# Kernel optimization log

Hardware: AMD Instinct MI355X
Metric: run time of the kernel (lower is better)

## Reference

```python
import jax, jax.numpy as jnp
import numpy as np
from jax import lax

N_WIRES = 4
# Deterministic stand-in for tq.RandomLayer(n_ops=50): fixed gate sequence.
_rng = np.random.RandomState(12345)
_GATES = ['rx', 'ry', 'rz', 'crx', 'cnot']
RAND_SPEC = []
for _ in range(50):
    g = _GATES[_rng.randint(len(_GATES))]
    if g in ('crx', 'cnot'):
        w = [int(v) for v in _rng.choice(N_WIRES, size=2, replace=False)]
    else:
        w = [int(_rng.randint(N_WIRES))]
    RAND_SPEC.append((g, w))
N_RAND_PARAMS = sum(1 for g, _ in RAND_SPEC if g != 'cnot')

C64 = jnp.complex64
H_MAT = (jnp.array([[1, 1], [1, -1]], C64) / np.float32(np.sqrt(2.0)))
SX_MAT = 0.5 * jnp.array([[1 + 1j, 1 - 1j], [1 - 1j, 1 + 1j]], C64)
CNOT_MAT = jnp.array([[1, 0, 0, 0], [0, 1, 0, 0], [0, 0, 0, 1], [0, 0, 1, 0]], C64)


def rx_mat(t):
    t = jnp.asarray(t, jnp.float32)
    c = jnp.cos(t / 2).astype(C64)
    js = (-1j) * jnp.sin(t / 2).astype(C64)
    return jnp.stack([jnp.stack([c, js], -1), jnp.stack([js, c], -1)], -2)


def ry_mat(t):
    t = jnp.asarray(t, jnp.float32)
    c = jnp.cos(t / 2).astype(C64)
    s = jnp.sin(t / 2).astype(C64)
    return jnp.stack([jnp.stack([c, -s], -1), jnp.stack([s, c], -1)], -2)


def rz_mat(t):
    t = jnp.asarray(t, jnp.float32).astype(C64)
    em = jnp.exp(-0.5j * t)
    ep = jnp.exp(0.5j * t)
    z = jnp.zeros_like(em)
    return jnp.stack([jnp.stack([em, z], -1), jnp.stack([z, ep], -1)], -2)


def crx_mat(t):
    r = rx_mat(t)  # [2,2]
    m = jnp.eye(4, dtype=C64)
    return m.at[2:, 2:].set(r)


def apply_1q(state, U, wire):
    # state: [B,2,2,2,2]; U: [2,2] or [B,2,2]
    st = jnp.moveaxis(state, wire + 1, 1)
    sh = st.shape
    st = st.reshape(sh[0], 2, -1)
    if U.ndim == 2:
        st = jnp.einsum('ij,bjk->bik', U, st)
    else:
        st = jnp.einsum('bij,bjk->bik', U, st)
    return jnp.moveaxis(st.reshape(sh), 1, wire + 1)


def apply_2q(state, U, w0, w1):
    # U: [4,4], basis |w0 w1>
    st = jnp.moveaxis(state, (w0 + 1, w1 + 1), (1, 2))
    sh = st.shape
    st = st.reshape(sh[0], 4, -1)
    st = jnp.einsum('ij,bjk->bik', U, st)
    return jnp.moveaxis(st.reshape(sh), (1, 2), (w0 + 1, w1 + 1))


def maxpool2(h):
    return lax.reduce_window(h, -jnp.inf, lax.max, (1, 1, 2, 2), (1, 1, 2, 2), 'VALID')


def conv2d_same(h, w, b):
    o = lax.conv_general_dilated(h, w, (1, 1), 'SAME', dimension_numbers=('NCHW', 'OIHW', 'NCHW'))
    return o + b[None, :, None, None]


def setup_inputs() -> dict:
    key = jax.random.key(0)
    ks = jax.random.split(key, 12)
    B = 8192
    inp = {}
    inp['x'] = jax.random.normal(ks[0], (B, 1, 28, 28), jnp.float32)
    inp['conv1_w'] = jax.random.normal(ks[1], (8, 1, 3, 3), jnp.float32) * 0.2
    inp['conv1_b'] = jax.random.normal(ks[2], (8,), jnp.float32) * 0.05
    inp['conv2_w'] = jax.random.normal(ks[3], (16, 8, 3, 3), jnp.float32) * 0.1
    inp['conv2_b'] = jax.random.normal(ks[4], (16,), jnp.float32) * 0.05
    inp['gate_params'] = jax.random.normal(ks[5], (4,), jnp.float32)  # rx0, ry0, rz0, crx0
    inp['rand_params'] = jax.random.normal(ks[6], (N_RAND_PARAMS,), jnp.float32)
    inp['bn_gamma'] = jnp.ones((4,), jnp.float32)
    inp['bn_beta'] = jnp.zeros((4,), jnp.float32)
    inp['fc_w'] = jax.random.normal(ks[7], (1, 4), jnp.float32) * 0.5
    inp['fc_b'] = jnp.zeros((1,), jnp.float32)
    return inp


def reference(x, conv1_w, conv1_b, conv2_w, conv2_b, gate_params, rand_params, bn_gamma, bn_beta, fc_w, fc_b):
    B = x.shape[0]
    # --- CNN feature extractor ---
    h = jax.nn.relu(conv2d_same(x, conv1_w, conv1_b))
    h = maxpool2(h)                       # [B,8,14,14]
    h = jax.nn.relu(conv2d_same(h, conv2_w, conv2_b))
    h = maxpool2(h)                       # [B,16,7,7]
    pooled = h.mean(axis=(2, 3))          # [B,16] -> rotation angles

    # --- quantum circuit on 4 wires, state [B,2,2,2,2], wire 0 = axis 1 ---
    state = jnp.zeros((B, 2, 2, 2, 2), C64).at[:, 0, 0, 0, 0].set(1.0)

    # GeneralEncoder '4x4_ryzxy': ry, rz, rx, ry over wires 0..3 with inputs 0..15
    idx = 0
    for f in (ry_mat, rz_mat, rx_mat, ry_mat):
        for w in range(N_WIRES):
            state = apply_1q(state, f(pooled[:, idx]), w)
            idx += 1

    # RandomLayer (frozen deterministic 50-op sequence)
    mat_of = {'rx': rx_mat, 'ry': ry_mat, 'rz': rz_mat}
    p = 0
    for g, wires in RAND_SPEC:
        if g == 'cnot':
            state = apply_2q(state, CNOT_MAT, wires[0], wires[1])
        elif g == 'crx':
            state = apply_2q(state, crx_mat(rand_params[p]), wires[0], wires[1])
            p += 1
        else:
            state = apply_1q(state, mat_of[g](rand_params[p]), wires[0])
            p += 1

    # fixed trainable gates + fixed gates
    state = apply_1q(state, rx_mat(gate_params[0]), 0)
    state = apply_1q(state, ry_mat(gate_params[1]), 1)
    state = apply_1q(state, rz_mat(gate_params[2]), 3)
    state = apply_2q(state, crx_mat(gate_params[3]), 0, 2)
    state = apply_1q(state, H_MAT, 3)
    state = apply_1q(state, SX_MAT, 2)
    state = apply_2q(state, CNOT_MAT, 3, 0)

    # MeasureAll(PauliZ): <Z_w> = p(bit_w=0) - p(bit_w=1)
    probs = state.real ** 2 + state.imag ** 2  # [B,2,2,2,2]
    zvec = jnp.array([1.0, -1.0], jnp.float32)
    exps = []
    for w in range(N_WIRES):
        pw = probs.sum(axis=tuple(a for a in range(1, 5) if a != w + 1))  # [B,2]
        exps.append(pw @ zvec)
    out = jnp.stack(exps, axis=1)  # [B,4]

    # BatchNorm1d (training-mode batch statistics, eps=1e-5)
    mu = out.mean(axis=0)
    var = out.var(axis=0)
    out = (out - mu) / jnp.sqrt(var + 1e-5) * bn_gamma + bn_beta

    # Linear classifier 4 -> 1
    return out @ fc_w.T + fc_b
```

## Files before the change

### kernel.cpp

```cpp
#include <hip/hip_runtime.h>
#include <hip/hip_bf16.h>
#include <hip/hip_fp16.h>
#include <cstdint>
#include <random>

typedef __attribute__((ext_vector_type(8))) short short8;
typedef __attribute__((ext_vector_type(4))) float floatx4;

#define NGMAX 60
struct GateSpec {
  unsigned char type[NGMAX];
  unsigned char w0[NGMAX];
  unsigned char w1[NGMAX];
  signed char   src[NGMAX];
  signed char   pidx[NGMAX];
  int n;
};

static GateSpec build_spec() {
  GateSpec sp; sp.n = 0;
  std::mt19937 mt(12345u);
  int p = 0;
  auto add = [&](int ty, int a, int b, int s, int pi) {
    sp.type[sp.n] = (unsigned char)ty; sp.w0[sp.n] = (unsigned char)a;
    sp.w1[sp.n] = (unsigned char)b; sp.src[sp.n] = (signed char)s;
    sp.pidx[sp.n] = (signed char)pi; sp.n++;
  };
  for (int op = 0; op < 50; ++op) {
    unsigned g;
    for (;;) { uint32_t v = mt() & 7u; if (v <= 4u) { g = v; break; } }
    if (g == 3u || g == 4u) {
      int arr[4] = {0, 1, 2, 3};
      for (int i = 3; i >= 1; --i) {
        uint32_t mask = (i == 1) ? 1u : 3u;
        uint32_t j;
        for (;;) { j = mt() & mask; if (j <= (uint32_t)i) break; }
        int t = arr[i]; arr[i] = arr[j]; arr[j] = t;
      }
      if (g == 3u) add(3, arr[0], arr[1], 0, p++);
      else         add(4, arr[0], arr[1], 2, -1);
    } else {
      int w = (int)(mt() & 3u);
      add((int)g, w, 0, 0, p++);
    }
  }
  add(0, 0, 0, 1, 0);
  add(1, 1, 0, 1, 1);
  add(2, 3, 0, 1, 2);
  add(3, 0, 2, 1, 3);
  add(5, 3, 0, 2, -1);
  add(6, 2, 0, 2, -1);
  add(4, 3, 0, 2, -1);
  return sp;
}

__device__ __forceinline__ float2 cmul(float2 a, float2 b) {
  return make_float2(fmaf(a.x, b.x, -a.y * b.y), fmaf(a.x, b.y, a.y * b.x));
}

__device__ __forceinline__ unsigned short f2bf(float f) {
  __hip_bfloat16 h = __float2bfloat16(f);
  return *reinterpret_cast<unsigned short*>(&h);
}

#define WS_BW   512
#define WS_W1C  1408
#define WS_O4   1456

__global__ void prep_kernel(const float* __restrict__ rp, const float* __restrict__ gp,
                            const float* __restrict__ c1w, const float* __restrict__ c1b,
                            const float* __restrict__ c2w,
                            float* __restrict__ ws, GateSpec sp) {
  const int tid = threadIdx.x;

  __hip_bfloat16* Bwg = (__hip_bfloat16*)(ws + WS_BW);
  __half2* w1cg = (__half2*)(ws + WS_W1C);
  for (int i = tid; i < 896; i += 256)
    ((unsigned int*)Bwg)[i] = 0u;
  __syncthreads();
  for (int i = tid; i < 1152; i += 256) {
    const int co = i / 72, rem = i - co * 72;
    const int ci = rem / 9, tap = rem - ci * 9;
    Bwg[co * 112 + tap * 8 + ci] = __float2bfloat16(c2w[i]);
  }
  if (tid < 40) {
    const int p = tid / 10, t = tid - p * 10;
    __half2 v;
    if (t < 9) v = __halves2half2(__float2half(c1w[(2 * p) * 9 + t]),
                                  __float2half(c1w[(2 * p + 1) * 9 + t]));
    else       v = __halves2half2(__float2half(c1b[2 * p]), __float2half(c1b[2 * p + 1]));
    w1cg[p * 12 + t] = v;
  }

  const int r = tid & 15;
  const int c = tid >> 4;
  float2 u = make_float2((r == c) ? 1.f : 0.f, 0.f);
  for (int g = 0; g < sp.n; ++g) {
    const int ty = sp.type[g];
    float th = 0.f;
    const int s = sp.src[g];
    if (s == 0) th = rp[(int)sp.pidx[g]];
    else if (s == 1) th = gp[(int)sp.pidx[g]];
    const float ch = cosf(th * 0.5f), sh = sinf(th * 0.5f);
    if (ty == 0) {
      const int m = 1 << (3 - sp.w0[g]);
      const float px_ = __shfl_xor(u.x, m), py_ = __shfl_xor(u.y, m);
      u = make_float2(fmaf(ch, u.x, sh * py_), fmaf(ch, u.y, -sh * px_));
    } else if (ty == 1) {
      const int bp = 3 - sp.w0[g]; const int m = 1 << bp; const int b = (r >> bp) & 1;
      const float px_ = __shfl_xor(u.x, m), py_ = __shfl_xor(u.y, m);
      const float sgn = b ? sh : -sh;
      u = make_float2(fmaf(ch, u.x, sgn * px_), fmaf(ch, u.y, sgn * py_));
    } else if (ty == 2) {
      const int bp = 3 - sp.w0[g]; const int b = (r >> bp) & 1;
      u = cmul(make_float2(ch, b ? sh : -sh), u);
    } else if (ty == 3) {
      const int bpc = 3 - sp.w0[g]; const int m = 1 << (3 - sp.w1[g]);
      const float px_ = __shfl_xor(u.x, m), py_ = __shfl_xor(u.y, m);
      if ((r >> bpc) & 1)
        u = make_float2(fmaf(ch, u.x, sh * py_), fmaf(ch, u.y, -sh * px_));
    } else if (ty == 4) {
      const int bpc = 3 - sp.w0[g]; const int m = 1 << (3 - sp.w1[g]);
      const float px_ = __shfl_xor(u.x, m), py_ = __shfl_xor(u.y, m);
      if ((r >> bpc) & 1) u = make_float2(px_, py_);
    } else if (ty == 5) {
      const int bp = 3 - sp.w0[g]; const int m = 1 << bp; const int b = (r >> bp) & 1;
      const float px_ = __shfl_xor(u.x, m), py_ = __shfl_xor(u.y, m);
      const float is2 = 0.70710678118654752f;
      u = b ? make_float2(is2 * (px_ - u.x), is2 * (py_ - u.y))
            : make_float2(is2 * (u.x + px_), is2 * (u.y + py_));
    } else {
      const int m = 1 << (3 - sp.w0[g]);
      const float px_ = __shfl_xor(u.x, m), py_ = __shfl_xor(u.y, m);
      u = make_float2(0.5f * (u.x - u.y + px_ + py_), 0.5f * (u.x + u.y + py_ - px_));
    }
  }
  ws[2 * (r * 16 + c) + 0] = u.x;
  ws[2 * (r * 16 + c) + 1] = u.y;
}

__global__ __launch_bounds__(256, 4) void cnn_quantum_kernel(
    const float* __restrict__ x,
    const float* __restrict__ c2b,
    const float* __restrict__ ws,
    float* __restrict__ o4, int B) {
  __shared__ __align__(16) __half2 sxp2[4 * 900];
  __shared__ __align__(16) unsigned short h1t[4 * 304 * 8];

  const int tid  = threadIdx.x;
  const int lane = tid & 63;
  const int wid  = tid >> 6;
  int img = blockIdx.x * 4 + wid;
  if (img >= B) img = B - 1;

  const float* __restrict__ Ug = ws;
  const __hip_bfloat16* __restrict__ Bwg = (const __hip_bfloat16*)(ws + WS_BW);
  const __half2* __restrict__ w1cg = (const __half2*)(ws + WS_W1C);

  __half2* swave = sxp2 + wid * 900;
  unsigned short* hwave = h1t + wid * 304 * 8;

  for (int i = lane; i < 116; i += 64) {
    int idx;
    if (i < 30) idx = i;
    else if (i < 60) idx = 870 + (i - 30);
    else { const int r = (i - 60) >> 1, c = (i - 60) & 1; idx = (r + 1) * 30 + (c ? 29 : 0); }
    swave[idx] = __float2half2_rn(0.f);
  }
  {
    const uint4 z4 = make_uint4(0u, 0u, 0u, 0u);
    uint4* h4 = (uint4*)hwave;
    for (int s = lane; s < 304; s += 64) h4[s] = z4;
  }
  const float* xb = x + (size_t)img * 784;
  for (int t = lane; t < 196; t += 64) {
    const float4 v4 = *(const float4*)(xb + 4 * t);
    const int yy = t / 7;
    const int xoff = 4 * (t - 7 * yy);
    __half2* dst = &swave[(yy + 1) * 30 + xoff + 1];
    dst[0] = __float2half2_rn(v4.x);
    dst[1] = __float2half2_rn(v4.y);
    dst[2] = __float2half2_rn(v4.z);
    dst[3] = __float2half2_rn(v4.w);
  }
  __syncthreads();

  {
    const int p = lane & 3;
    const int grp = lane >> 2;
    const __half2* __restrict__ wrow = w1cg + p * 12;
    __half2 wr[9];
#pragma unroll
    for (int k = 0; k < 9; ++k) wr[k] = wrow[k];
    const __half2 bias = wrow[9];
    for (int s = grp; s < 196; s += 16) {
      const int py = s / 14, px = s - py * 14;
      const int base = 2 * (py * 30 + px);
      __half2 q[4][4];
#pragma unroll
      for (int j = 0; j < 4; ++j) {
        const __half2* rowp = &swave[base + j * 30];
        q[j][0] = rowp[0]; q[j][1] = rowp[1]; q[j][2] = rowp[2]; q[j][3] = rowp[3];
      }
      __half2 s00 = bias, s01 = bias, s10 = bias, s11 = bias;
#pragma unroll
      for (int ky = 0; ky < 3; ++ky)
#pragma unroll
        for (int kx = 0; kx < 3; ++kx) {
          const __half2 w = wr[ky * 3 + kx];
          s00 = __hfma2(q[ky][kx], w, s00);
          s01 = __hfma2(q[ky][kx + 1], w, s01);
          s10 = __hfma2(q[ky + 1][kx], w, s10);
          s11 = __hfma2(q[ky + 1][kx + 1], w, s11);
        }
      const float lo = fmaxf(fmaxf(fmaxf(__low2float(s00), __low2float(s01)),
                                   fmaxf(__low2float(s10), __low2float(s11))), 0.f);
      const float hi = fmaxf(fmaxf(fmaxf(__high2float(s00), __high2float(s01)),
                                   fmaxf(__high2float(s10), __high2float(s11))), 0.f);
      const int site = (py + 1) * 16 + (px + 1);
      const unsigned int pk = (unsigned int)f2bf(lo) | ((unsigned int)f2bf(hi) << 16);
      *(unsigned int*)&hwave[site * 8 + 2 * p] = pk;
    }
  }
  __syncthreads();

  float asum = 0.f;
  {
    const int n = lane & 15;
    const int g = lane >> 4;

    short8 bfrag[3];
#pragma unroll
    for (int kt = 0; kt < 3; ++kt)
      bfrag[kt] = *(const short8*)&Bwg[n * 112 + kt * 32 + g * 8];
    const float bias2 = c2b[n];

    for (int t = 0; t < 13; ++t) {
      const int m = lane & 15;
      const int S = t * 16 + m;
      const int p = S >> 2, q = S & 3;
      const int p7 = p / 7;
      const int py = 2 * p7 + (q >> 1);
      const int px = 2 * (p - 7 * p7) + (q & 1);
      floatx4 acc = {0.f, 0.f, 0.f, 0.f};
#pragma unroll
      for (int kt = 0; kt < 3; ++kt) {
        const int tap = kt * 4 + g;
        const int dy = tap / 3, dx = tap - 3 * dy;
        const short8 a = *(const short8*)&hwave[((py + dy) * 16 + (px + dx)) * 8];
        acc = __builtin_amdgcn_mfma_f32_16x16x32_bf16(a, bfrag[kt], acc, 0, 0, 0);
      }
      const int pq = t * 4 + g;
      if (pq < 49) {
        const float v = fmaxf(fmaxf(acc[0], acc[1]), fmaxf(acc[2], acc[3]));
        asum += fmaxf(v + bias2, 0.f);
      }
    }
    asum += __shfl_xor(asum, 16);
    asum += __shfl_xor(asum, 32);
  }

  const float angw = asum * (1.0f / 49.0f);

  const int w = lane & 3;
  const float a0 = __shfl(angw, w);
  const float a1 = __shfl(angw, 4 + w);
  const float a2 = __shfl(angw, 8 + w);
  const float a3 = __shfl(angw, 12 + w);
  float c0, s0; sincosf(a0 * 0.5f, &s0, &c0);
  float2 v0 = make_float2(c0, 0.f), v1 = make_float2(s0, 0.f);
  float c1, s1; sincosf(a1 * 0.5f, &s1, &c1);
  v0 = cmul(make_float2(c1, -s1), v0);
  v1 = cmul(make_float2(c1, s1), v1);
  float c2, s2; sincosf(a2 * 0.5f, &s2, &c2);
  const float2 iv0 = make_float2(-v0.y, v0.x);
  const float2 iv1 = make_float2(-v1.y, v1.x);
  const float2 nv0 = make_float2(c2 * v0.x - s2 * iv1.x, c2 * v0.y - s2 * iv1.y);
  const float2 nv1 = make_float2(c2 * v1.x - s2 * iv0.x, c2 * v1.y - s2 * iv0.y);
  float c3, s3; sincosf(a3 * 0.5f, &s3, &c3);
  v0 = make_float2(c3 * nv0.x - s3 * nv1.x, c3 * nv0.y - s3 * nv1.y);
  v1 = make_float2(s3 * nv0.x + c3 * nv1.x, s3 * nv0.y + c3 * nv1.y);

  const int t16 = lane & 15;
  float2 psi = make_float2(1.f, 0.f);
#pragma unroll
  for (int ww = 0; ww < 4; ++ww) {
    const float g0x = __shfl(v0.x, ww), g0y = __shfl(v0.y, ww);
    const float g1x = __shfl(v1.x, ww), g1y = __shfl(v1.y, ww);
    const int bb = (t16 >> (3 - ww)) & 1;
    const float2 vw = bb ? make_float2(g1x, g1y) : make_float2(g0x, g0y);
    psi = cmul(psi, vw);
  }

  const float2* __restrict__ Uc = (const float2*)Ug;
  float2 accp = make_float2(0.f, 0.f);
#pragma unroll
  for (int j = 0; j < 16; ++j) {
    const float2 uu = Uc[t16 * 16 + j];
    const float ppx = __shfl(psi.x, j), ppy = __shfl(psi.y, j);
    accp.x = fmaf(uu.x, ppx, accp.x); accp.x = fmaf(-uu.y, ppy, accp.x);
    accp.y = fmaf(uu.x, ppy, accp.y); accp.y = fmaf(uu.y, ppx, accp.y);
  }
  const float pr = accp.x * accp.x + accp.y * accp.y;

  float e0 = (t16 & 8) ? -pr : pr;
  float e1 = (t16 & 4) ? -pr : pr;
  float e2 = (t16 & 2) ? -pr : pr;
  float e3 = (t16 & 1) ? -pr : pr;
#pragma unroll
  for (int m = 1; m <= 8; m <<= 1) {
    e0 += __shfl_xor(e0, m); e1 += __shfl_xor(e1, m);
    e2 += __shfl_xor(e2, m); e3 += __shfl_xor(e3, m);
  }
  if (lane == 0) {
    float4 r; r.x = e0; r.y = e1; r.z = e2; r.w = e3;
    *(float4*)(o4 + (size_t)img * 4) = r;
  }
}

__global__ __launch_bounds__(1024) void bn_fc_kernel(
    const float* __restrict__ o4, const float* __restrict__ gamma,
    const float* __restrict__ beta, const float* __restrict__ fcw,
    const float* __restrict__ fcb, float* __restrict__ out, int B) {
  __shared__ float redS[16][8];
  __shared__ float coef[5];
  const int tid = threadIdx.x;
  float s0 = 0, s1 = 0, s2 = 0, s3 = 0, q0 = 0, q1 = 0, q2 = 0, q3 = 0;
  for (int r = tid; r < B; r += 1024) {
    const float4 v = *(const float4*)(o4 + (size_t)r * 4);
    s0 += v.x; s1 += v.y; s2 += v.z; s3 += v.w;
    q0 += v.x * v.x; q1 += v.y * v.y; q2 += v.z * v.z; q3 += v.w * v.w;
  }
#pragma unroll
  for (int off = 32; off > 0; off >>= 1) {
    s0 += __shfl_down(s0, off); s1 += __shfl_down(s1, off);
    s2 += __shfl_down(s2, off); s3 += __shfl_down(s3, off);
    q0 += __shfl_down(q0, off); q1 += __shfl_down(q1, off);
    q2 += __shfl_down(q2, off); q3 += __shfl_down(q3, off);
  }
  const int wv = tid >> 6, ln = tid & 63;
  if (ln == 0) {
    redS[wv][0] = s0; redS[wv][1] = s1; redS[wv][2] = s2; redS[wv][3] = s3;
    redS[wv][4] = q0; redS[wv][5] = q1; redS[wv][6] = q2; redS[wv][7] = q3;
  }
  __syncthreads();
  if (tid == 0) {
    float S[8] = {0, 0, 0, 0, 0, 0, 0, 0};
    for (int w = 0; w < 16; ++w)
      for (int k = 0; k < 8; ++k) S[k] += redS[w][k];
    float C = fcb[0];
    for (int k = 0; k < 4; ++k) {
      const float mu = S[k] / (float)B;
      const float var = S[4 + k] / (float)B - mu * mu;
      const float rstd = 1.0f / sqrtf(var + 1e-5f);
      coef[k] = fcw[k] * gamma[k] * rstd;
      C += fcw[k] * (beta[k] - mu * rstd * gamma[k]);
    }
    coef[4] = C;
  }
  __syncthreads();
  const float A0 = coef[0], A1 = coef[1], A2 = coef[2], A3 = coef[3], Cc = coef[4];
  const int r = blockIdx.x * 256 + tid;
  if (tid < 256 && r < B) {
    const float4 v = *(const float4*)(o4 + (size_t)r * 4);
    out[r] = Cc + A0 * v.x + A1 * v.y + A2 * v.z + A3 * v.w;
  }
}

extern "C" void kernel_launch(void* const* d_in, const int* in_sizes, int n_in,
                              void* d_out, int out_size, void* d_ws, size_t ws_size,
                              hipStream_t stream) {
  const float* x   = (const float*)d_in[0];
  const float* c1w = (const float*)d_in[1];
  const float* c1b = (const float*)d_in[2];
  const float* c2w = (const float*)d_in[3];
  const float* c2b = (const float*)d_in[4];
  const float* gp  = (const float*)d_in[5];
  const float* rp  = (const float*)d_in[6];
  const float* gam = (const float*)d_in[7];
  const float* bet = (const float*)d_in[8];
  const float* fcw = (const float*)d_in[9];
  const float* fcb = (const float*)d_in[10];
  float* out = (float*)d_out;
  const int B = in_sizes[0] / 784;

  float* ws = (float*)d_ws;
  float* o4 = ws + WS_O4;

  GateSpec sp = build_spec();
  prep_kernel<<<1, 256, 0, stream>>>(rp, gp, c1w, c1b, c2w, ws, sp);
  const int nblk = (B + 3) / 4;
  cnn_quantum_kernel<<<nblk, 256, 0, stream>>>(x, c2b, ws, o4, B);
  const int nfin = (B + 255) / 256;
  bn_fc_kernel<<<nfin, 1024, 0, stream>>>(o4, gam, bet, fcw, fcb, out, B);
}
```

Before: 148.7 us.

## Fuse batchnorm and classifier into main kernel via last-block ticket

Removes the separate bn_fc kernel launch and folds its work into the main CNN/quantum kernel. Each block increments an atomic ticket counter after writing its outputs, and the last block to finish computes the batch statistics and the final linear outputs for the whole batch. This saves one kernel launch and its gap. In exchange, the final reduction and output pass run serially on a single 256-thread block instead of many 1024-thread blocks, which could be slow for a large batch.

```diff
diff --git a/kernel.cpp b/kernel.cpp
--- a/kernel.cpp
+++ b/kernel.cpp
@@ -65,13 +65,16 @@
 
 #define WS_BW   512
 #define WS_W1C  1408
-#define WS_O4   1456
+#define WS_TKT  1456
+#define WS_O4   1460
 
 __global__ void prep_kernel(const float* __restrict__ rp, const float* __restrict__ gp,
                             const float* __restrict__ c1w, const float* __restrict__ c1b,
                             const float* __restrict__ c2w,
                             float* __restrict__ ws, GateSpec sp) {
   const int tid = threadIdx.x;
+
+  if (tid == 0) *(int*)(ws + WS_TKT) = 0;
 
   __hip_bfloat16* Bwg = (__hip_bfloat16*)(ws + WS_BW);
   __half2* w1cg = (__half2*)(ws + WS_W1C);
@@ -142,10 +145,16 @@
 __global__ __launch_bounds__(256, 4) void cnn_quantum_kernel(
     const float* __restrict__ x,
     const float* __restrict__ c2b,
-    const float* __restrict__ ws,
-    float* __restrict__ o4, int B) {
+    float* __restrict__ ws,
+    float* __restrict__ o4,
+    const float* __restrict__ gamma, const float* __restrict__ beta,
+    const float* __restrict__ fcw, const float* __restrict__ fcb,
+    float* __restrict__ out, int B) {
   __shared__ __align__(16) __half2 sxp2[4 * 900];
   __shared__ __align__(16) unsigned short h1t[4 * 304 * 8];
+  __shared__ int lastFlag;
+  __shared__ float redS[4][8];
+  __shared__ float coef[5];
 
   const int tid  = threadIdx.x;
   const int lane = tid & 63;
@@ -316,54 +325,55 @@
     float4 r; r.x = e0; r.y = e1; r.z = e2; r.w = e3;
     *(float4*)(o4 + (size_t)img * 4) = r;
   }
-}
-
-__global__ __launch_bounds__(1024) void bn_fc_kernel(
-    const float* __restrict__ o4, const float* __restrict__ gamma,
-    const float* __restrict__ beta, const float* __restrict__ fcw,
-    const float* __restrict__ fcb, float* __restrict__ out, int B) {
-  __shared__ float redS[16][8];
-  __shared__ float coef[5];
-  const int tid = threadIdx.x;
-  float s0 = 0, s1 = 0, s2 = 0, s3 = 0, q0 = 0, q1 = 0, q2 = 0, q3 = 0;
-  for (int r = tid; r < B; r += 1024) {
-    const float4 v = *(const float4*)(o4 + (size_t)r * 4);
-    s0 += v.x; s1 += v.y; s2 += v.z; s3 += v.w;
-    q0 += v.x * v.x; q1 += v.y * v.y; q2 += v.z * v.z; q3 += v.w * v.w;
-  }
-#pragma unroll
-  for (int off = 32; off > 0; off >>= 1) {
-    s0 += __shfl_down(s0, off); s1 += __shfl_down(s1, off);
-    s2 += __shfl_down(s2, off); s3 += __shfl_down(s3, off);
-    q0 += __shfl_down(q0, off); q1 += __shfl_down(q1, off);
-    q2 += __shfl_down(q2, off); q3 += __shfl_down(q3, off);
-  }
-  const int wv = tid >> 6, ln = tid & 63;
-  if (ln == 0) {
-    redS[wv][0] = s0; redS[wv][1] = s1; redS[wv][2] = s2; redS[wv][3] = s3;
-    redS[wv][4] = q0; redS[wv][5] = q1; redS[wv][6] = q2; redS[wv][7] = q3;
-  }
+
   __syncthreads();
   if (tid == 0) {
-    float S[8] = {0, 0, 0, 0, 0, 0, 0, 0};
-    for (int w = 0; w < 16; ++w)
-      for (int k = 0; k < 8; ++k) S[k] += redS[w][k];
-    float C = fcb[0];
-    for (int k = 0; k < 4; ++k) {
-      const float mu = S[k] / (float)B;
-      const float var = S[4 + k] / (float)B - mu * mu;
-      const float rstd = 1.0f / sqrtf(var + 1e-5f);
-      coef[k] = fcw[k] * gamma[k] * rstd;
-      C += fcw[k] * (beta[k] - mu * rstd * gamma[k]);
-    }
-    coef[4] = C;
+    __threadfence();
+    int* tkt = (int*)(ws + WS_TKT);
+    const int ticket = atomicAdd(tkt, 1);
+    lastFlag = (ticket == (int)gridDim.x - 1);
+    if (lastFlag) __threadfence();
   }
   __syncthreads();
-  const float A0 = coef[0], A1 = coef[1], A2 = coef[2], A3 = coef[3], Cc = coef[4];
-  const int r = blockIdx.x * 256 + tid;
-  if (tid < 256 && r < B) {
-    const float4 v = *(const float4*)(o4 + (size_t)r * 4);
-    out[r] = Cc + A0 * v.x + A1 * v.y + A2 * v.z + A3 * v.w;
+  if (lastFlag) {
+    float s0 = 0, s1 = 0, s2 = 0, s3 = 0, q0 = 0, q1 = 0, q2 = 0, q3 = 0;
+    for (int r = tid; r < B; r += 256) {
+      const float4 v = *(const float4*)(o4 + (size_t)r * 4);
+      s0 += v.x; s1 += v.y; s2 += v.z; s3 += v.w;
+      q0 += v.x * v.x; q1 += v.y * v.y; q2 += v.z * v.z; q3 += v.w * v.w;
+    }
+#pragma unroll
+    for (int off = 32; off > 0; off >>= 1) {
+      s0 += __shfl_down(s0, off); s1 += __shfl_down(s1, off);
+      s2 += __shfl_down(s2, off); s3 += __shfl_down(s3, off);
+      q0 += __shfl_down(q0, off); q1 += __shfl_down(q1, off);
+      q2 += __shfl_down(q2, off); q3 += __shfl_down(q3, off);
+    }
+    if (lane == 0) {
+      redS[wid][0] = s0; redS[wid][1] = s1; redS[wid][2] = s2; redS[wid][3] = s3;
+      redS[wid][4] = q0; redS[wid][5] = q1; redS[wid][6] = q2; redS[wid][7] = q3;
+    }
+    __syncthreads();
+    if (tid == 0) {
+      float S[8] = {0, 0, 0, 0, 0, 0, 0, 0};
+      for (int wv = 0; wv < 4; ++wv)
+        for (int k = 0; k < 8; ++k) S[k] += redS[wv][k];
+      float C = fcb[0];
+      for (int k = 0; k < 4; ++k) {
+        const float mu = S[k] / (float)B;
+        const float var = S[4 + k] / (float)B - mu * mu;
+        const float rstd = 1.0f / sqrtf(var + 1e-5f);
+        coef[k] = fcw[k] * gamma[k] * rstd;
+        C += fcw[k] * (beta[k] - mu * rstd * gamma[k]);
+      }
+      coef[4] = C;
+    }
+    __syncthreads();
+    const float A0 = coef[0], A1 = coef[1], A2 = coef[2], A3 = coef[3], Cc = coef[4];
+    for (int r = tid; r < B; r += 256) {
+      const float4 v = *(const float4*)(o4 + (size_t)r * 4);
+      out[r] = Cc + A0 * v.x + A1 * v.y + A2 * v.z + A3 * v.w;
+    }
   }
 }
 
@@ -390,7 +400,5 @@
   GateSpec sp = build_spec();
   prep_kernel<<<1, 256, 0, stream>>>(rp, gp, c1w, c1b, c2w, ws, sp);
   const int nblk = (B + 3) / 4;
-  cnn_quantum_kernel<<<nblk, 256, 0, stream>>>(x, c2b, ws, o4, B);
-  const int nfin = (B + 255) / 256;
-  bn_fc_kernel<<<nfin, 1024, 0, stream>>>(o4, gam, bet, fcw, fcb, out, B);
-}
+  cnn_quantum_kernel<<<nblk, 256, 0, stream>>>(x, c2b, ws, o4, gam, bet, fcw, fcb, out, B);
+}
```

New measurement: 190.5 us. 1.28x slower.
